# Kernel tuning notes

Measured on AMD Instinct MI355X. Metric: run time of the kernel, lower is better.

## Reference

```python
import jax, jax.numpy as jnp
import numpy as np

D_MODEL = 1024
N_HEADS = 16
D_HEAD = D_MODEL // N_HEADS
B, S = 2, 2048


def setup_inputs() -> dict:
    key = jax.random.key(0)
    ks = jax.random.split(key, 14)
    std = 0.02
    inp = {
        "query": jax.random.normal(ks[0], (B, S, D_MODEL), dtype=jnp.float32),
        "key": jax.random.normal(ks[1], (B, S, D_MODEL), dtype=jnp.float32),
        "value": jax.random.normal(ks[2], (B, S, D_MODEL), dtype=jnp.float32),
        "mask": jax.random.randint(ks[3], (B, 1, S, S), 0, 2, dtype=jnp.int32),
        "position_bias": jax.random.normal(ks[4], (1, N_HEADS, S, S), dtype=jnp.float32),
        "w_q": jax.random.normal(ks[5], (D_MODEL, D_MODEL), dtype=jnp.float32) * std,
        "b_q": jnp.zeros((D_MODEL,), dtype=jnp.float32),
        "w_k": jax.random.normal(ks[6], (D_MODEL, D_MODEL), dtype=jnp.float32) * std,
        "b_k": jnp.zeros((D_MODEL,), dtype=jnp.float32),
        "w_v": jax.random.normal(ks[7], (D_MODEL, D_MODEL), dtype=jnp.float32) * std,
        "b_v": jnp.zeros((D_MODEL,), dtype=jnp.float32),
        "w_o": jax.random.normal(ks[8], (D_MODEL, D_MODEL), dtype=jnp.float32) * std,
        "b_o": jnp.zeros((D_MODEL,), dtype=jnp.float32),
    }
    return inp


def reference(query, key, value, mask, position_bias,
              w_q, b_q, w_k, b_k, w_v, b_v, w_o, b_o):
    b = query.shape[0]
    # projections: torch Linear computes x @ W^T + b
    def proj(x, w, bias):
        y = x @ w.T + bias                       # [b, s, D]
        return y.reshape(b, -1, N_HEADS, D_HEAD).transpose(0, 2, 1, 3)  # [b, h, s, d]

    Q = proj(query, w_q, b_q)
    K = proj(key, w_k, b_k)
    V = proj(value, w_v, b_v)

    scale = 1.0 / jnp.sqrt(jnp.asarray(D_HEAD, dtype=Q.dtype))
    scores = jnp.einsum("bhqd,bhkd->bhqk", Q, K) * scale
    scores = scores + position_bias
    scores = jnp.where(mask == 0, jnp.asarray(-1e9, dtype=scores.dtype), scores)
    attn = jax.nn.softmax(scores, axis=-1)       # dropout is identity at eval
    ctx = jnp.einsum("bhqk,bhkd->bhqd", attn, V)  # [b, h, s, d]
    ctx = ctx.transpose(0, 2, 1, 3).reshape(b, -1, N_HEADS * D_HEAD)
    return ctx @ w_o.T + b_o
```

## Files before the change

kernel.cpp:

```cpp
#include <hip/hip_runtime.h>
#include <hip/hip_bf16.h>

#define S_LEN 2048
#define DM 1024
#define NH 16
#define DH 64
#define MTOK 4096

typedef __attribute__((ext_vector_type(8))) __bf16 bf16x8;
typedef __attribute__((ext_vector_type(4))) float f32x4;
typedef __attribute__((ext_vector_type(16))) float f32x16;
typedef unsigned short u16;
typedef unsigned long long u64;

__device__ __forceinline__ u16 f2bf(float f) {
  union { float f; unsigned u; } a; a.f = f;
  unsigned u = a.u;
  u += 0x7fffu + ((u >> 16) & 1u);
  return (u16)(u >> 16);
}

__device__ __forceinline__ bf16x8 ld_bf8(const u16* p) {
  return *reinterpret_cast<const bf16x8*>(p);
}

__global__ void k_convert(const float* __restrict__ src, u16* __restrict__ dst, int n4) {
  int i = blockIdx.x * blockDim.x + threadIdx.x;
  int stride = gridDim.x * blockDim.x;
  for (; i < n4; i += stride) {
    float4 v = reinterpret_cast<const float4*>(src)[i];
    ushort4 o;
    o.x = f2bf(v.x); o.y = f2bf(v.y); o.z = f2bf(v.z); o.w = f2bf(v.w);
    reinterpret_cast<ushort4*>(dst)[i] = o;
  }
}

__global__ void k_maskpack(const int* __restrict__ m, u64* __restrict__ o, int n) {
  int i = blockIdx.x * blockDim.x + threadIdx.x;
  int stride = gridDim.x * blockDim.x;
  for (; i < n; i += stride) {
    u64 bal = __ballot(m[i] != 0);
    if ((i & 63) == 0) o[i >> 6] = bal;
  }
}

template<int MODE>
__global__ __launch_bounds__(256) void k_gemm(
    const u16* __restrict__ A, const u16* __restrict__ Bw,
    const float* __restrict__ bias, void* __restrict__ dst) {
  constexpr int K = DM;
  __shared__ u16 As[128 * 32];
  __shared__ u16 Bs[128 * 32];
  const int tid = threadIdx.x;
  const int lane = tid & 63;
  const int wid = tid >> 6;
  const int wm = wid >> 1, wn = wid & 1;
  const int bm = blockIdx.x * 128;
  const int bn = blockIdx.y * 128;
  const int r0 = tid >> 2;
  const int c0 = (tid & 3) * 8;
  const int fr = lane & 15;
  const int fk = (lane >> 4) * 8;

  f32x4 acc[4][4] = {};

  const u16* ga = A + (size_t)(bm + r0) * K + c0;
  const u16* gb = Bw + (size_t)(bn + r0) * K + c0;

  for (int kt = 0; kt < K; kt += 32) {
    __syncthreads();
    __builtin_amdgcn_global_load_lds(
        (const __attribute__((address_space(1))) void*)(ga + kt),
        (__attribute__((address_space(3))) void*)(&As[r0 * 32 + c0]), 16, 0, 0);
    __builtin_amdgcn_global_load_lds(
        (const __attribute__((address_space(1))) void*)(ga + (size_t)64 * K + kt),
        (__attribute__((address_space(3))) void*)(&As[(r0 + 64) * 32 + c0]), 16, 0, 0);
    __builtin_amdgcn_global_load_lds(
        (const __attribute__((address_space(1))) void*)(gb + kt),
        (__attribute__((address_space(3))) void*)(&Bs[r0 * 32 + c0]), 16, 0, 0);
    __builtin_amdgcn_global_load_lds(
        (const __attribute__((address_space(1))) void*)(gb + (size_t)64 * K + kt),
        (__attribute__((address_space(3))) void*)(&Bs[(r0 + 64) * 32 + c0]), 16, 0, 0);
    __syncthreads();
    bf16x8 af[4], bfr[4];
#pragma unroll
    for (int m = 0; m < 4; ++m) af[m] = ld_bf8(&As[(wm * 64 + m * 16 + fr) * 32 + fk]);
#pragma unroll
    for (int n = 0; n < 4; ++n) bfr[n] = ld_bf8(&Bs[(wn * 64 + n * 16 + fr) * 32 + fk]);
#pragma unroll
    for (int m = 0; m < 4; ++m)
#pragma unroll
      for (int n = 0; n < 4; ++n)
        acc[m][n] = __builtin_amdgcn_mfma_f32_16x16x32_bf16(af[m], bfr[n], acc[m][n], 0, 0, 0);
  }

  const int cr = (lane >> 4) * 4;
  const int cc = lane & 15;
#pragma unroll
  for (int m = 0; m < 4; ++m) {
#pragma unroll
    for (int n = 0; n < 4; ++n) {
      const int colg = bn + wn * 64 + n * 16 + cc;
      const float bv = bias[colg];
      const int rbase = bm + wm * 64 + m * 16 + cr;
      if (MODE == 2) {
        float* o = (float*)dst;
#pragma unroll
        for (int r = 0; r < 4; ++r)
          o[(size_t)(rbase + r) * DM + colg] = acc[m][n][r] + bv;
      } else if (MODE == 0) {
        u16* o = (u16*)dst;
        const int h = colg >> 6, d = colg & 63;
#pragma unroll
        for (int r = 0; r < 4; ++r) {
          const int tok = rbase + r;
          const int b = tok >> 11, s = tok & 2047;
          o[(((size_t)(b * NH + h) * S_LEN) + s) * DH + d] = f2bf(acc[m][n][r] + bv);
        }
      } else {
        u16* o = (u16*)dst;
        const int h = colg >> 6, d = colg & 63;
        const int tok = rbase;
        const int b = tok >> 11, s = tok & 2047;
        ushort4 pk;
        pk.x = f2bf(acc[m][n][0] + bv);
        pk.y = f2bf(acc[m][n][1] + bv);
        pk.z = f2bf(acc[m][n][2] + bv);
        pk.w = f2bf(acc[m][n][3] + bv);
        *reinterpret_cast<ushort4*>(&o[(((size_t)(b * NH + h) * DH) + d) * S_LEN + s]) = pk;
      }
    }
  }
}

__global__ __launch_bounds__(256, 2) void k_attn(
    const u16* __restrict__ Qb, const u16* __restrict__ Kb, const u16* __restrict__ Vt,
    const float* __restrict__ bias, const u64* __restrict__ mpk,
    u16* __restrict__ ctx) {
  __shared__ u16 lds[2][4][4096];
  const int tid = threadIdx.x;
  const int lane = tid & 63;
  const int w = tid >> 6;
  const int b = w >> 1;
  const int h = blockIdx.y;
  const int q0 = blockIdx.x * 64 + (w & 1) * 32;
  const int lq = lane & 31;
  const int hi = lane >> 5;

  const float* bp = bias + (size_t)h * S_LEN * S_LEN;

  bf16x8 qf[4];
  f32x16 cacc[2] = {};
  float m_run = -1e30f, l_run = 0.f;
  {
    const u16* Qp = Qb + (size_t)(b * NH + h) * S_LEN * DH;
#pragma unroll
    for (int d0 = 0; d0 < 4; ++d0)
      qf[d0] = ld_bf8(&Qp[(size_t)(q0 + lq) * DH + d0 * 16 + hi * 8]);
  }

#define STAGE(ktv, cb) {                                                          \
    _Pragma("unroll") for (int i = 0; i < 2; ++i) {                               \
      const int el = (i * 256 + tid) * 8;                                         \
      const int rr = el >> 6;                                                     \
      const int ce = ((tid & 7) * 8) ^ ((rr & 7) << 3);                           \
      _Pragma("unroll") for (int b2 = 0; b2 < 2; ++b2) {                          \
        const u16* ksrc = Kb + (size_t)(b2 * NH + h) * S_LEN * DH                 \
                          + (size_t)((ktv) + rr) * DH + ce;                       \
        const u16* vsrc = Vt + (size_t)(b2 * NH + h) * DH * S_LEN                 \
                          + (size_t)rr * S_LEN + (ktv) + ce;                      \
        __builtin_amdgcn_global_load_lds(                                         \
            (const __attribute__((address_space(1))) void*)ksrc,                  \
            (__attribute__((address_space(3))) void*)&lds[cb][b2][el], 16, 0, 0); \
        __builtin_amdgcn_global_load_lds(                                         \
            (const __attribute__((address_space(1))) void*)vsrc,                  \
            (__attribute__((address_space(3))) void*)&lds[cb][2 + b2][el], 16, 0, 0); \
      } } }

#define LDSREAD(cb, tile, row, cel) \
    ld_bf8(&lds[cb][tile][(row) * 64 + (((cel)) ^ (((row) & 7) << 3))])

#define LOADB(BV, ktv) {                                                          \
    _Pragma("unroll") for (int kb = 0; kb < 2; ++kb)                              \
      _Pragma("unroll") for (int rq = 0; rq < 4; ++rq)                            \
        BV[kb][rq] = *reinterpret_cast<const float4*>(                            \
            &bp[(size_t)(q0 + lq) * S_LEN + (ktv) + kb * 32 + rq * 8 + hi * 4]); }

#define BODY(T, BV, BVN) {                                                        \
    const int ktv = (T) * 64;                                                     \
    __syncthreads();                                                              \
    if ((T) + 1 < S_LEN / 64) { STAGE(ktv + 64, c ^ 1); LOADB(BVN, ktv + 64); }   \
    const u64 mw = mpk[((size_t)(b * S_LEN + q0 + lq)) * 32 + (ktv >> 6)];        \
    f32x16 sc0 = {}, sc1 = {};                                                    \
    _Pragma("unroll") for (int d0 = 0; d0 < 4; ++d0) {                            \
      bf16x8 ka0 = LDSREAD(c, b, lq, d0 * 16 + hi * 8);                           \
      sc0 = __builtin_amdgcn_mfma_f32_32x32x16_bf16(ka0, qf[d0], sc0, 0, 0, 0);   \
      bf16x8 ka1 = LDSREAD(c, b, 32 + lq, d0 * 16 + hi * 8);                      \
      sc1 = __builtin_amdgcn_mfma_f32_32x32x16_bf16(ka1, qf[d0], sc1, 0, 0, 0);   \
    }                                                                             \
    _Pragma("unroll") for (int r = 0; r < 16; ++r) {                              \
      const int cr_ = (r & 3) + 8 * (r >> 2);                                     \
      const float v0_ = sc0[r] * 0.125f + ((const float*)&BV[0][r >> 2])[r & 3];  \
      sc0[r] = ((mw >> (cr_ + 4 * hi)) & 1) ? v0_ : -1e9f;                        \
      const float v1_ = sc1[r] * 0.125f + ((const float*)&BV[1][r >> 2])[r & 3];  \
      sc1[r] = ((mw >> (32 + cr_ + 4 * hi)) & 1) ? v1_ : -1e9f;                   \
    }                                                                             \
    float vm = fmaxf(sc0[0], sc1[0]);                                             \
    _Pragma("unroll") for (int r = 1; r < 16; ++r)                                \
      vm = fmaxf(vm, fmaxf(sc0[r], sc1[r]));                                      \
    vm = fmaxf(vm, __shfl_xor(vm, 32));                                           \
    if (!__all(vm <= m_run)) {                                                    \
      const float mn = fmaxf(m_run, vm);                                          \
      const float corr = __expf(m_run - mn);                                      \
      m_run = mn;                                                                 \
      l_run *= corr;                                                              \
      _Pragma("unroll") for (int r = 0; r < 16; ++r) {                            \
        cacc[0][r] *= corr; cacc[1][r] *= corr; }                                 \
    }                                                                             \
    float ssum = 0.f;                                                             \
    _Pragma("unroll") for (int r = 0; r < 16; ++r) {                              \
      const float p0 = __expf(sc0[r] - m_run); sc0[r] = p0;                       \
      const float p1 = __expf(sc1[r] - m_run); sc1[r] = p1;                       \
      ssum += p0 + p1;                                                            \
    }                                                                             \
    ssum += __shfl_xor(ssum, 32);                                                 \
    l_run += ssum;                                                                \
    unsigned pw0[8], pw1[8];                                                      \
    _Pragma("unroll") for (int i2 = 0; i2 < 8; ++i2) {                            \
      pw0[i2] = (unsigned)f2bf(sc0[2 * i2]) | ((unsigned)f2bf(sc0[2 * i2 + 1]) << 16); \
      pw1[i2] = (unsigned)f2bf(sc1[2 * i2]) | ((unsigned)f2bf(sc1[2 * i2 + 1]) << 16); \
    }                                                                             \
    bf16x8 pf[4];                                                                 \
    _Pragma("unroll") for (int kb = 0; kb < 2; ++kb)                              \
      _Pragma("unroll") for (int ch = 0; ch < 2; ++ch) {                          \
        const unsigned a0 = kb ? pw1[ch * 4 + 0] : pw0[ch * 4 + 0];               \
        const unsigned a1 = kb ? pw1[ch * 4 + 1] : pw0[ch * 4 + 1];               \
        const unsigned a2 = kb ? pw1[ch * 4 + 2] : pw0[ch * 4 + 2];               \
        const unsigned a3 = kb ? pw1[ch * 4 + 3] : pw0[ch * 4 + 3];               \
        const unsigned sx0 = __shfl_xor(a0, 32), sx1 = __shfl_xor(a1, 32);        \
        const unsigned sx2 = __shfl_xor(a2, 32), sx3 = __shfl_xor(a3, 32);        \
        union { unsigned u[4]; bf16x8 v; } f;                                     \
        f.u[0] = hi ? sx2 : a0;                                                   \
        f.u[1] = hi ? sx3 : a1;                                                   \
        f.u[2] = hi ? a2 : sx0;                                                   \
        f.u[3] = hi ? a3 : sx1;                                                   \
        pf[kb * 2 + ch] = f.v;                                                    \
      }                                                                           \
    _Pragma("unroll") for (int db = 0; db < 2; ++db)                              \
      _Pragma("unroll") for (int kc = 0; kc < 4; ++kc) {                          \
        bf16x8 va = LDSREAD(c, 2 + b, db * 32 + lq, kc * 16 + hi * 8);            \
        cacc[db] = __builtin_amdgcn_mfma_f32_32x32x16_bf16(va, pf[kc], cacc[db], 0, 0, 0); \
      }                                                                           \
    c ^= 1;                                                                       \
  }

  float4 bvA[2][4], bvB[2][4];
  STAGE(0, 0);
  LOADB(bvA, 0);
  int c = 0;
  for (int t0 = 0; t0 < S_LEN / 64; t0 += 2) {
    BODY(t0, bvA, bvB);
    BODY(t0 + 1, bvB, bvA);
  }
#undef STAGE
#undef LDSREAD
#undef LOADB
#undef BODY

  {
    const float linv = 1.0f / l_run;
    u16* cp = ctx + ((size_t)(b * S_LEN + q0 + lq)) * DM + h * DH;
#pragma unroll
    for (int db = 0; db < 2; ++db)
#pragma unroll
      for (int r = 0; r < 16; ++r)
        cp[db * 32 + (r & 3) + 8 * (r >> 2) + 4 * hi] = f2bf(cacc[db][r] * linv);
  }
}

extern "C" void kernel_launch(void* const* d_in, const int* in_sizes, int n_in,
                              void* d_out, int out_size, void* d_ws, size_t ws_size,
                              hipStream_t stream) {
  const float* q   = (const float*)d_in[0];
  const float* k   = (const float*)d_in[1];
  const float* v   = (const float*)d_in[2];
  const int*   msk = (const int*)d_in[3];
  const float* pb  = (const float*)d_in[4];
  const float* w_q = (const float*)d_in[5];
  const float* b_q = (const float*)d_in[6];
  const float* w_k = (const float*)d_in[7];
  const float* b_k = (const float*)d_in[8];
  const float* w_v = (const float*)d_in[9];
  const float* b_v = (const float*)d_in[10];
  const float* w_o = (const float*)d_in[11];
  const float* b_o = (const float*)d_in[12];
  float* out = (float*)d_out;

  char* ws = (char*)d_ws;
  u16* wq_bf = (u16*)(ws + ((size_t)0 << 20));
  u16* wk_bf = (u16*)(ws + ((size_t)2 << 20));
  u16* wv_bf = (u16*)(ws + ((size_t)4 << 20));
  u16* wo_bf = (u16*)(ws + ((size_t)6 << 20));
  u16* x_bf  = (u16*)(ws + ((size_t)8 << 20));
  u16* Qb    = (u16*)(ws + ((size_t)16 << 20));
  u16* Kb    = (u16*)(ws + ((size_t)24 << 20));
  u16* Vtb   = (u16*)(ws + ((size_t)32 << 20));
  u64* mpk   = (u64*)(ws + ((size_t)40 << 20));

  dim3 blk(256);
  const int n4w = DM * DM / 4;
  const int n4x = MTOK * DM / 4;
  k_convert<<<dim3(1024), blk, 0, stream>>>(w_q, wq_bf, n4w);
  k_convert<<<dim3(1024), blk, 0, stream>>>(w_k, wk_bf, n4w);
  k_convert<<<dim3(1024), blk, 0, stream>>>(w_v, wv_bf, n4w);
  k_convert<<<dim3(1024), blk, 0, stream>>>(w_o, wo_bf, n4w);
  k_maskpack<<<dim3(2048), blk, 0, stream>>>(msk, mpk, 2 * S_LEN * S_LEN);

  dim3 gg(32, 8);
  k_convert<<<dim3(2048), blk, 0, stream>>>(q, x_bf, n4x);
  k_gemm<0><<<gg, blk, 0, stream>>>(x_bf, wq_bf, b_q, Qb);
  k_convert<<<dim3(2048), blk, 0, stream>>>(k, x_bf, n4x);
  k_gemm<0><<<gg, blk, 0, stream>>>(x_bf, wk_bf, b_k, Kb);
  k_convert<<<dim3(2048), blk, 0, stream>>>(v, x_bf, n4x);
  k_gemm<1><<<gg, blk, 0, stream>>>(x_bf, wv_bf, b_v, Vtb);

  k_attn<<<dim3(32, NH), blk, 0, stream>>>(Qb, Kb, Vtb, pb, mpk, x_bf);
  k_gemm<2><<<gg, blk, 0, stream>>>(x_bf, wo_bf, b_o, out);
}
```

Measured before the change: 287.4 us.

## Prefetch mask words, use partial vmcnt barrier, raise MFMA priority

```diff
diff --git a/kernel.cpp b/kernel.cpp
--- a/kernel.cpp
+++ b/kernel.cpp
@@ -186,24 +186,36 @@
         BV[kb][rq] = *reinterpret_cast<const float4*>(                            \
             &bp[(size_t)(q0 + lq) * S_LEN + (ktv) + kb * 32 + rq * 8 + hi * 4]); }
 
-#define BODY(T, BV, BVN) {                                                        \
+#define BARRIER() {                                                               \
+    asm volatile("s_waitcnt vmcnt(9) lgkmcnt(0)" ::: "memory");                   \
+    __builtin_amdgcn_sched_barrier(0);                                            \
+    __builtin_amdgcn_s_barrier();                                                 \
+    __builtin_amdgcn_sched_barrier(0); }
+
+#define BODY(T, BV, MW, BVN, MWN) {                                               \
     const int ktv = (T) * 64;                                                     \
-    __syncthreads();                                                              \
-    if ((T) + 1 < S_LEN / 64) { STAGE(ktv + 64, c ^ 1); LOADB(BVN, ktv + 64); }   \
-    const u64 mw = mpk[((size_t)(b * S_LEN + q0 + lq)) * 32 + (ktv >> 6)];        \
+    BARRIER();                                                                    \
+    if ((T) + 1 < S_LEN / 64) {                                                   \
+      STAGE(ktv + 64, c ^ 1);                                                     \
+      __builtin_amdgcn_sched_barrier(0);                                          \
+      LOADB(BVN, ktv + 64);                                                       \
+      MWN = mpk[((size_t)(b * S_LEN + q0 + lq)) * 32 + (ktv >> 6) + 1];           \
+    }                                                                             \
     f32x16 sc0 = {}, sc1 = {};                                                    \
+    __builtin_amdgcn_s_setprio(1);                                                \
     _Pragma("unroll") for (int d0 = 0; d0 < 4; ++d0) {                            \
       bf16x8 ka0 = LDSREAD(c, b, lq, d0 * 16 + hi * 8);                           \
       sc0 = __builtin_amdgcn_mfma_f32_32x32x16_bf16(ka0, qf[d0], sc0, 0, 0, 0);   \
       bf16x8 ka1 = LDSREAD(c, b, 32 + lq, d0 * 16 + hi * 8);                      \
       sc1 = __builtin_amdgcn_mfma_f32_32x32x16_bf16(ka1, qf[d0], sc1, 0, 0, 0);   \
     }                                                                             \
+    __builtin_amdgcn_s_setprio(0);                                                \
     _Pragma("unroll") for (int r = 0; r < 16; ++r) {                              \
       const int cr_ = (r & 3) + 8 * (r >> 2);                                     \
       const float v0_ = sc0[r] * 0.125f + ((const float*)&BV[0][r >> 2])[r & 3];  \
-      sc0[r] = ((mw >> (cr_ + 4 * hi)) & 1) ? v0_ : -1e9f;                        \
+      sc0[r] = ((MW >> (cr_ + 4 * hi)) & 1) ? v0_ : -1e9f;                        \
       const float v1_ = sc1[r] * 0.125f + ((const float*)&BV[1][r >> 2])[r & 3];  \
-      sc1[r] = ((mw >> (32 + cr_ + 4 * hi)) & 1) ? v1_ : -1e9f;                   \
+      sc1[r] = ((MW >> (32 + cr_ + 4 * hi)) & 1) ? v1_ : -1e9f;                   \
     }                                                                             \
     float vm = fmaxf(sc0[0], sc1[0]);                                             \
     _Pragma("unroll") for (int r = 1; r < 16; ++r)                                \
@@ -246,25 +258,31 @@
         f.u[3] = hi ? a3 : sx1;                                                   \
         pf[kb * 2 + ch] = f.v;                                                    \
       }                                                                           \
+    __builtin_amdgcn_s_setprio(1);                                                \
     _Pragma("unroll") for (int db = 0; db < 2; ++db)                              \
       _Pragma("unroll") for (int kc = 0; kc < 4; ++kc) {                          \
         bf16x8 va = LDSREAD(c, 2 + b, db * 32 + lq, kc * 16 + hi * 8);            \
         cacc[db] = __builtin_amdgcn_mfma_f32_32x32x16_bf16(va, pf[kc], cacc[db], 0, 0, 0); \
       }                                                                           \
+    __builtin_amdgcn_s_setprio(0);                                                \
     c ^= 1;                                                                       \
   }
 
   float4 bvA[2][4], bvB[2][4];
+  u64 mwA, mwB;
   STAGE(0, 0);
+  __builtin_amdgcn_sched_barrier(0);
   LOADB(bvA, 0);
+  mwA = mpk[((size_t)(b * S_LEN + q0 + lq)) * 32];
   int c = 0;
   for (int t0 = 0; t0 < S_LEN / 64; t0 += 2) {
-    BODY(t0, bvA, bvB);
-    BODY(t0 + 1, bvB, bvA);
+    BODY(t0, bvA, mwA, bvB, mwB);
+    BODY(t0 + 1, bvB, mwB, bvA, mwA);
   }
 #undef STAGE
 #undef LDSREAD
 #undef LOADB
+#undef BARRIER
 #undef BODY
 
   {
```

After: 283.7 us. About the same (-1.3%).
